# Performance work log

Measured on AMD Instinct MI355X. Metric: run time of the kernel, lower is better.

The kernel has to match this reference:

```python
import jax, jax.numpy as jnp
import numpy as np

N, IN_F, OUT_F = 10000, 512, 64
ALPHA = 0.2       # leaky relu slope
THRESHOLD = 0.01  # hub threshold
NEG_INF = -9.0e15


def setup_inputs() -> dict:
    key = jax.random.key(0)
    k_h, k_adj, k_hub, k_W, k_as, k_ad = jax.random.split(key, 6)
    h = jax.random.normal(k_h, (N, IN_F), dtype=jnp.float32)
    adj = jax.random.randint(k_adj, (N, N), 0, 2, dtype=jnp.int32)
    hub_mask = jax.random.uniform(k_hub, (N,), dtype=jnp.float32)
    # xavier-uniform-ish params (gain 1.414)
    lim_W = 1.414 * np.sqrt(6.0 / (IN_F + OUT_F))
    W = jax.random.uniform(k_W, (IN_F, OUT_F), minval=-lim_W, maxval=lim_W, dtype=jnp.float32)
    lim_a = 1.414 * np.sqrt(6.0 / (OUT_F + 1))
    a_src = jax.random.uniform(k_as, (OUT_F, 1), minval=-lim_a, maxval=lim_a, dtype=jnp.float32)
    a_dst = jax.random.uniform(k_ad, (OUT_F, 1), minval=-lim_a, maxval=lim_a, dtype=jnp.float32)
    return {"h": h, "W": W, "a_src": a_src, "a_dst": a_dst, "hub_mask": hub_mask, "adj": adj}


def reference(h, W, a_src, a_dst, hub_mask, adj):
    Wh = h @ W                                  # [N, F_out]
    e_src = Wh @ a_src                          # [N, 1]
    e_dst = Wh @ a_dst                          # [N, 1]
    e = jax.nn.leaky_relu(e_src + e_dst.T, negative_slope=ALPHA)  # [N, N]
    scores = jnp.where(adj > 0, e, jnp.float32(NEG_INF))
    attention = jax.nn.softmax(scores, axis=1)  # row-wise softmax over neighbors
    attention = jax.nn.relu(attention - hub_mask * THRESHOLD)  # hub threshold prune
    # dropout omitted (inference mode / p applied as no-op for deterministic reference)
    h_prime = attention @ Wh                    # [N, F_out]
    return jax.nn.elu(h_prime)                  # concat=True branch
```

## Files before the change

kernel.cpp:

```cpp
#include <hip/hip_runtime.h>
#include <math.h>

#define N_NODES 10000
#define IN_FEAT 512
#define OUT_FEAT 64
#define LRELU_ALPHA 0.2f
#define HUB_THRESH 0.01f
#define BITS_WORDS 320
#define CAND_CAP 1024

#define WH_OFF   0
#define ESRC_OFF 640000
#define EDST_OFF 650000
#define T_OFF    660000
#define LT_OFF   670000

__global__ __launch_bounds__(256) void k1_gemm(
    const float* __restrict__ h, const float* __restrict__ W,
    const float* __restrict__ a_src, const float* __restrict__ a_dst,
    const float* __restrict__ hub, float* __restrict__ ws)
{
    const int bx = blockIdx.x, tid = threadIdx.x;
    if (bx >= 625) {
        const int base = (bx - 625) * 1024;
        #pragma unroll
        for (int e = 0; e < 4; ++e) {
            int idx = base + e * 256 + tid;
            if (idx < N_NODES) {
                float t = hub[idx] * HUB_THRESH;
                ws[T_OFF + idx]  = t;
                ws[LT_OFF + idx] = logf(t);
            }
        }
        return;
    }

    __shared__ __align__(16) float Ws[64 * 64];
    __shared__ __align__(16) float Hs[16 * 64];
    const int col = tid & 63, rg = tid >> 6;
    const int rowBase = bx * 16;
    float acc[4] = {0.f, 0.f, 0.f, 0.f};

    for (int k0 = 0; k0 < IN_FEAT; k0 += 64) {
        for (int idx = tid; idx < 4096; idx += 256) {
            int kk = idx >> 6, c = idx & 63;
            Ws[idx] = W[(size_t)(k0 + kk) * 64 + c];
        }
        for (int idx = tid; idx < 1024; idx += 256) {
            int r = idx >> 6, kk = idx & 63;
            Hs[idx] = h[(size_t)(rowBase + r) * IN_FEAT + k0 + kk];
        }
        __syncthreads();
        #pragma unroll
        for (int k4 = 0; k4 < 16; ++k4) {
            float4 hv0 = *(const float4*)&Hs[(rg + 0)  * 64 + k4 * 4];
            float4 hv1 = *(const float4*)&Hs[(rg + 4)  * 64 + k4 * 4];
            float4 hv2 = *(const float4*)&Hs[(rg + 8)  * 64 + k4 * 4];
            float4 hv3 = *(const float4*)&Hs[(rg + 12) * 64 + k4 * 4];
            float w0 = Ws[(k4 * 4 + 0) * 64 + col];
            float w1 = Ws[(k4 * 4 + 1) * 64 + col];
            float w2 = Ws[(k4 * 4 + 2) * 64 + col];
            float w3 = Ws[(k4 * 4 + 3) * 64 + col];
            acc[0] += hv0.x * w0 + hv0.y * w1 + hv0.z * w2 + hv0.w * w3;
            acc[1] += hv1.x * w0 + hv1.y * w1 + hv1.z * w2 + hv1.w * w3;
            acc[2] += hv2.x * w0 + hv2.y * w1 + hv2.z * w2 + hv2.w * w3;
            acc[3] += hv3.x * w0 + hv3.y * w1 + hv3.z * w2 + hv3.w * w3;
        }
        __syncthreads();
    }

    const float asv = a_src[col], adv = a_dst[col];
    #pragma unroll
    for (int r = 0; r < 4; ++r) {
        int row = rowBase + rg + 4 * r;
        ws[WH_OFF + (size_t)row * 64 + col] = acc[r];
        float s1 = acc[r] * asv, s2 = acc[r] * adv;
        #pragma unroll
        for (int m = 32; m; m >>= 1) {
            s1 += __shfl_xor(s1, m, 64);
            s2 += __shfl_xor(s2, m, 64);
        }
        if (col == 0) {
            ws[ESRC_OFF + row] = s1;
            ws[EDST_OFF + row] = s2;
        }
    }
}

__global__ __launch_bounds__(256) void k2_fused(
    const int* __restrict__ adj, const float* __restrict__ ws,
    float* __restrict__ out)
{
    const int i = blockIdx.x, tid = threadIdx.x;
    const int lane = tid & 63, w = tid >> 6;
    __shared__ unsigned bits[BITS_WORDS];
    __shared__ float partA[4];
    __shared__ float partB[256];
    __shared__ int   candj[2][CAND_CAP];
    __shared__ float candw[2][CAND_CAP];
    __shared__ int   cnt[10];

    const float esrc = ws[ESRC_OFF + i];
    const float* __restrict__ edst = ws + EDST_OFF;
    const int4* __restrict__ arow = (const int4*)(adj + (size_t)i * N_NODES);
    float acc = 0.f;

    if (tid < 10) cnt[tid] = 0;

    #pragma unroll
    for (int it = 0; it < 10; ++it) {
        const int j0 = it * 1024 + tid * 4;
        unsigned nib = 0;
        if (j0 < N_NODES) {
            int4 a4  = arow[j0 >> 2];
            float4 e4 = *(const float4*)(edst + j0);
            float s, e;
            s = esrc + e4.x; e = fmaxf(s, LRELU_ALPHA * s);
            if (a4.x > 0) { acc += __expf(e); nib |= 1u; }
            s = esrc + e4.y; e = fmaxf(s, LRELU_ALPHA * s);
            if (a4.y > 0) { acc += __expf(e); nib |= 2u; }
            s = esrc + e4.z; e = fmaxf(s, LRELU_ALPHA * s);
            if (a4.z > 0) { acc += __expf(e); nib |= 4u; }
            s = esrc + e4.w; e = fmaxf(s, LRELU_ALPHA * s);
            if (a4.w > 0) { acc += __expf(e); nib |= 8u; }
        }
        unsigned v = nib << ((lane & 7) * 4);
        v |= (unsigned)__shfl_xor((int)v, 1, 64);
        v |= (unsigned)__shfl_xor((int)v, 2, 64);
        v |= (unsigned)__shfl_xor((int)v, 4, 64);
        if ((lane & 7) == 0) bits[j0 >> 5] = v;
    }

    #pragma unroll
    for (int m = 32; m; m >>= 1) acc += __shfl_xor(acc, m, 64);
    if (lane == 0) partA[w] = acc;
    __syncthreads();
    const float l = partA[0] + partA[1] + partA[2] + partA[3];

    const bool empty = (l == 0.0f);
    const float cl = empty ? 0.0f : logf(l);
    const float invN = 1.0f / (float)N_NODES;
    const float thr = cl - 0.0625f;
    const float* __restrict__ tarr  = ws + T_OFF;
    const float* __restrict__ ltarr = ws + LT_OFF;
    const float* __restrict__ Wh    = ws + WH_OFF;
    float oacc = 0.f;

    for (int it = 0; it < 10; ++it) {
        const int buf = it & 1;
        const int j0 = it * 1024 + tid * 4;
        if (j0 < N_NODES) {
            if (!empty) {
                const unsigned word = bits[j0 >> 5];
                const unsigned nib = (word >> (j0 & 31)) & 0xFu;
                if (nib) {
                    float4 e4  = *(const float4*)(edst + j0);
                    float4 lt4 = *(const float4*)(ltarr + j0);
                    #pragma unroll
                    for (int c = 0; c < 4; ++c) {
                        if (nib & (1u << c)) {
                            float ed = (c == 0) ? e4.x : (c == 1) ? e4.y : (c == 2) ? e4.z : e4.w;
                            float lt = (c == 0) ? lt4.x : (c == 1) ? lt4.y : (c == 2) ? lt4.z : lt4.w;
                            float s = esrc + ed;
                            float e = fmaxf(s, LRELU_ALPHA * s);
                            if (e > thr + lt) {
                                float p = __expf(e - cl);
                                float wgt = p - tarr[j0 + c];
                                if (wgt > 0.0f) {
                                    int k = atomicAdd(&cnt[it], 1);
                                    candj[buf][k] = j0 + c;
                                    candw[buf][k] = wgt;
                                }
                            }
                        }
                    }
                }
            } else {
                float4 t4 = *(const float4*)(tarr + j0);
                #pragma unroll
                for (int c = 0; c < 4; ++c) {
                    float tv = (c == 0) ? t4.x : (c == 1) ? t4.y : (c == 2) ? t4.z : t4.w;
                    float wgt = invN - tv;
                    if (wgt > 0.0f) {
                        int k = atomicAdd(&cnt[it], 1);
                        candj[buf][k] = j0 + c;
                        candw[buf][k] = wgt;
                    }
                }
            }
        }
        __syncthreads();
        const int M = cnt[it];
        for (int c = w; c < M; c += 4) {
            int   jj = candj[buf][c];
            float wv = candw[buf][c];
            oacc += wv * Wh[(size_t)jj * 64 + lane];
        }
    }

    partB[tid] = oacc;
    __syncthreads();
    if (w == 0) {
        float tot = partB[lane] + partB[64 + lane] + partB[128 + lane] + partB[192 + lane];
        out[(size_t)i * 64 + lane] = tot > 0.0f ? tot : expm1f(tot);
    }
}

extern "C" void kernel_launch(void* const* d_in, const int* in_sizes, int n_in,
                              void* d_out, int out_size, void* d_ws, size_t ws_size,
                              hipStream_t stream)
{
    const float* h     = (const float*)d_in[0];
    const float* W     = (const float*)d_in[1];
    const float* a_src = (const float*)d_in[2];
    const float* a_dst = (const float*)d_in[3];
    const float* hub   = (const float*)d_in[4];
    const int*   adj   = (const int*)d_in[5];
    float* ws  = (float*)d_ws;
    float* out = (float*)d_out;

    k1_gemm<<<635, 256, 0, stream>>>(h, W, a_src, a_dst, hub, ws);
    k2_fused<<<N_NODES, 256, 0, stream>>>(adj, ws, out);
}
```

Measured before the change: 655.1 us.

## Process two attention rows per block to share edst, threshold and Wh loads

Each block of the fused softmax/aggregation kernel now handles two adjacent rows, so the edst, log-threshold and threshold vectors are loaded once for both rows, and the grid is halved. Candidate index and weight are packed into one int2 array, and the candidate buffers are single-buffered with an extra barrier per iteration. The intent is to amortise the per-row shared vector traffic and block launch overhead. In exchange, per-block register and shared-memory use grows and there are half as many blocks.

```diff
diff --git a/kernel.cpp b/kernel.cpp
--- a/kernel.cpp
+++ b/kernel.cpp
@@ -91,118 +91,162 @@
     const int* __restrict__ adj, const float* __restrict__ ws,
     float* __restrict__ out)
 {
-    const int i = blockIdx.x, tid = threadIdx.x;
+    const int b = blockIdx.x, tid = threadIdx.x;
     const int lane = tid & 63, w = tid >> 6;
-    __shared__ unsigned bits[BITS_WORDS];
-    __shared__ float partA[4];
-    __shared__ float partB[256];
-    __shared__ int   candj[2][CAND_CAP];
-    __shared__ float candw[2][CAND_CAP];
-    __shared__ int   cnt[10];
-
-    const float esrc = ws[ESRC_OFF + i];
+    const int i0 = 2 * b, i1 = 2 * b + 1;
+    __shared__ unsigned bits[2][BITS_WORDS];
+    __shared__ float partA[2][4];
+    __shared__ int2  cand[2][CAND_CAP];
+    __shared__ int   cnt[2][10];
+
+    const float esrc0 = ws[ESRC_OFF + i0];
+    const float esrc1 = ws[ESRC_OFF + i1];
     const float* __restrict__ edst = ws + EDST_OFF;
-    const int4* __restrict__ arow = (const int4*)(adj + (size_t)i * N_NODES);
-    float acc = 0.f;
-
-    if (tid < 10) cnt[tid] = 0;
-
-    #pragma unroll
+    const int4* __restrict__ arow0 = (const int4*)(adj + (size_t)i0 * N_NODES);
+    const int4* __restrict__ arow1 = (const int4*)(adj + (size_t)i1 * N_NODES);
+    float acc0 = 0.f, acc1 = 0.f;
+
+    if (tid < 20) ((int*)cnt)[tid] = 0;
+
+    #pragma unroll 2
     for (int it = 0; it < 10; ++it) {
         const int j0 = it * 1024 + tid * 4;
-        unsigned nib = 0;
+        unsigned nib0 = 0, nib1 = 0;
         if (j0 < N_NODES) {
-            int4 a4  = arow[j0 >> 2];
+            int4 a0 = arow0[j0 >> 2];
+            int4 a1 = arow1[j0 >> 2];
             float4 e4 = *(const float4*)(edst + j0);
             float s, e;
-            s = esrc + e4.x; e = fmaxf(s, LRELU_ALPHA * s);
-            if (a4.x > 0) { acc += __expf(e); nib |= 1u; }
-            s = esrc + e4.y; e = fmaxf(s, LRELU_ALPHA * s);
-            if (a4.y > 0) { acc += __expf(e); nib |= 2u; }
-            s = esrc + e4.z; e = fmaxf(s, LRELU_ALPHA * s);
-            if (a4.z > 0) { acc += __expf(e); nib |= 4u; }
-            s = esrc + e4.w; e = fmaxf(s, LRELU_ALPHA * s);
-            if (a4.w > 0) { acc += __expf(e); nib |= 8u; }
-        }
-        unsigned v = nib << ((lane & 7) * 4);
-        v |= (unsigned)__shfl_xor((int)v, 1, 64);
-        v |= (unsigned)__shfl_xor((int)v, 2, 64);
-        v |= (unsigned)__shfl_xor((int)v, 4, 64);
-        if ((lane & 7) == 0) bits[j0 >> 5] = v;
+            s = esrc0 + e4.x; e = fmaxf(s, LRELU_ALPHA * s);
+            if (a0.x > 0) { acc0 += __expf(e); nib0 |= 1u; }
+            s = esrc0 + e4.y; e = fmaxf(s, LRELU_ALPHA * s);
+            if (a0.y > 0) { acc0 += __expf(e); nib0 |= 2u; }
+            s = esrc0 + e4.z; e = fmaxf(s, LRELU_ALPHA * s);
+            if (a0.z > 0) { acc0 += __expf(e); nib0 |= 4u; }
+            s = esrc0 + e4.w; e = fmaxf(s, LRELU_ALPHA * s);
+            if (a0.w > 0) { acc0 += __expf(e); nib0 |= 8u; }
+            s = esrc1 + e4.x; e = fmaxf(s, LRELU_ALPHA * s);
+            if (a1.x > 0) { acc1 += __expf(e); nib1 |= 1u; }
+            s = esrc1 + e4.y; e = fmaxf(s, LRELU_ALPHA * s);
+            if (a1.y > 0) { acc1 += __expf(e); nib1 |= 2u; }
+            s = esrc1 + e4.z; e = fmaxf(s, LRELU_ALPHA * s);
+            if (a1.z > 0) { acc1 += __expf(e); nib1 |= 4u; }
+            s = esrc1 + e4.w; e = fmaxf(s, LRELU_ALPHA * s);
+            if (a1.w > 0) { acc1 += __expf(e); nib1 |= 8u; }
+        }
+        unsigned v0 = nib0 << ((lane & 7) * 4);
+        unsigned v1 = nib1 << ((lane & 7) * 4);
+        v0 |= (unsigned)__shfl_xor((int)v0, 1, 64);
+        v1 |= (unsigned)__shfl_xor((int)v1, 1, 64);
+        v0 |= (unsigned)__shfl_xor((int)v0, 2, 64);
+        v1 |= (unsigned)__shfl_xor((int)v1, 2, 64);
+        v0 |= (unsigned)__shfl_xor((int)v0, 4, 64);
+        v1 |= (unsigned)__shfl_xor((int)v1, 4, 64);
+        if ((lane & 7) == 0) {
+            bits[0][j0 >> 5] = v0;
+            bits[1][j0 >> 5] = v1;
+        }
     }
 
     #pragma unroll
-    for (int m = 32; m; m >>= 1) acc += __shfl_xor(acc, m, 64);
-    if (lane == 0) partA[w] = acc;
+    for (int m = 32; m; m >>= 1) {
+        acc0 += __shfl_xor(acc0, m, 64);
+        acc1 += __shfl_xor(acc1, m, 64);
+    }
+    if (lane == 0) { partA[0][w] = acc0; partA[1][w] = acc1; }
     __syncthreads();
-    const float l = partA[0] + partA[1] + partA[2] + partA[3];
-
-    const bool empty = (l == 0.0f);
-    const float cl = empty ? 0.0f : logf(l);
+    const float l0 = partA[0][0] + partA[0][1] + partA[0][2] + partA[0][3];
+    const float l1 = partA[1][0] + partA[1][1] + partA[1][2] + partA[1][3];
+
+    const bool empty0 = (l0 == 0.0f), empty1 = (l1 == 0.0f);
+    const float cl0 = empty0 ? 0.0f : logf(l0);
+    const float cl1 = empty1 ? 0.0f : logf(l1);
+    const float thr0 = cl0 - 0.0625f, thr1 = cl1 - 0.0625f;
     const float invN = 1.0f / (float)N_NODES;
-    const float thr = cl - 0.0625f;
     const float* __restrict__ tarr  = ws + T_OFF;
     const float* __restrict__ ltarr = ws + LT_OFF;
     const float* __restrict__ Wh    = ws + WH_OFF;
-    float oacc = 0.f;
+    float oacc0 = 0.f, oacc1 = 0.f;
 
     for (int it = 0; it < 10; ++it) {
-        const int buf = it & 1;
         const int j0 = it * 1024 + tid * 4;
+        unsigned m0 = 0, m1 = 0;
         if (j0 < N_NODES) {
-            if (!empty) {
-                const unsigned word = bits[j0 >> 5];
-                const unsigned nib = (word >> (j0 & 31)) & 0xFu;
-                if (nib) {
-                    float4 e4  = *(const float4*)(edst + j0);
-                    float4 lt4 = *(const float4*)(ltarr + j0);
-                    #pragma unroll
-                    for (int c = 0; c < 4; ++c) {
-                        if (nib & (1u << c)) {
-                            float ed = (c == 0) ? e4.x : (c == 1) ? e4.y : (c == 2) ? e4.z : e4.w;
-                            float lt = (c == 0) ? lt4.x : (c == 1) ? lt4.y : (c == 2) ? lt4.z : lt4.w;
-                            float s = esrc + ed;
-                            float e = fmaxf(s, LRELU_ALPHA * s);
-                            if (e > thr + lt) {
-                                float p = __expf(e - cl);
-                                float wgt = p - tarr[j0 + c];
-                                if (wgt > 0.0f) {
-                                    int k = atomicAdd(&cnt[it], 1);
-                                    candj[buf][k] = j0 + c;
-                                    candw[buf][k] = wgt;
-                                }
-                            }
+            m0 = empty0 ? 0u : (bits[0][j0 >> 5] >> (j0 & 31)) & 0xFu;
+            m1 = empty1 ? 0u : (bits[1][j0 >> 5] >> (j0 & 31)) & 0xFu;
+        }
+        if (m0 | m1) {
+            float4 e4  = *(const float4*)(edst + j0);
+            float4 lt4 = *(const float4*)(ltarr + j0);
+            #pragma unroll
+            for (int c = 0; c < 4; ++c) {
+                float ed = (c == 0) ? e4.x  : (c == 1) ? e4.y  : (c == 2) ? e4.z  : e4.w;
+                float lt = (c == 0) ? lt4.x : (c == 1) ? lt4.y : (c == 2) ? lt4.z : lt4.w;
+                if (m0 & (1u << c)) {
+                    float s = esrc0 + ed;
+                    float e = fmaxf(s, LRELU_ALPHA * s);
+                    if (e > thr0 + lt) {
+                        float p = __expf(e - cl0);
+                        float wgt = p - tarr[j0 + c];
+                        if (wgt > 0.0f) {
+                            int k = atomicAdd(&cnt[0][it], 1);
+                            cand[0][k] = make_int2(j0 + c, __float_as_int(wgt));
                         }
                     }
                 }
-            } else {
-                float4 t4 = *(const float4*)(tarr + j0);
-                #pragma unroll
-                for (int c = 0; c < 4; ++c) {
-                    float tv = (c == 0) ? t4.x : (c == 1) ? t4.y : (c == 2) ? t4.z : t4.w;
-                    float wgt = invN - tv;
-                    if (wgt > 0.0f) {
-                        int k = atomicAdd(&cnt[it], 1);
-                        candj[buf][k] = j0 + c;
-                        candw[buf][k] = wgt;
+                if (m1 & (1u << c)) {
+                    float s = esrc1 + ed;
+                    float e = fmaxf(s, LRELU_ALPHA * s);
+                    if (e > thr1 + lt) {
+                        float p = __expf(e - cl1);
+                        float wgt = p - tarr[j0 + c];
+                        if (wgt > 0.0f) {
+                            int k = atomicAdd(&cnt[1][it], 1);
+                            cand[1][k] = make_int2(j0 + c, __float_as_int(wgt));
+                        }
                     }
                 }
             }
         }
-        __syncthreads();
-        const int M = cnt[it];
-        for (int c = w; c < M; c += 4) {
-            int   jj = candj[buf][c];
-            float wv = candw[buf][c];
-            oacc += wv * Wh[(size_t)jj * 64 + lane];
-        }
-    }
-
-    partB[tid] = oacc;
+        if ((empty0 | empty1) && j0 < N_NODES) {
+            float4 t4 = *(const float4*)(tarr + j0);
+            #pragma unroll
+            for (int c = 0; c < 4; ++c) {
+                float tv = (c == 0) ? t4.x : (c == 1) ? t4.y : (c == 2) ? t4.z : t4.w;
+                float wv = invN - tv;
+                if (wv > 0.0f) {
+                    if (empty0) {
+                        int k = atomicAdd(&cnt[0][it], 1);
+                        cand[0][k] = make_int2(j0 + c, __float_as_int(wv));
+                    }
+                    if (empty1) {
+                        int k = atomicAdd(&cnt[1][it], 1);
+                        cand[1][k] = make_int2(j0 + c, __float_as_int(wv));
+                    }
+                }
+            }
+        }
+        __syncthreads();
+        const int M0 = cnt[0][it], M1 = cnt[1][it];
+        for (int c = w; c < M0; c += 4) {
+            int2 cd = cand[0][c];
+            oacc0 += __int_as_float(cd.y) * Wh[(size_t)cd.x * 64 + lane];
+        }
+        for (int c = w; c < M1; c += 4) {
+            int2 cd = cand[1][c];
+            oacc1 += __int_as_float(cd.y) * Wh[(size_t)cd.x * 64 + lane];
+        }
+        __syncthreads();
+    }
+
+    float* partB = (float*)bits;
+    partB[tid]       = oacc0;
+    partB[256 + tid] = oacc1;
     __syncthreads();
-    if (w == 0) {
-        float tot = partB[lane] + partB[64 + lane] + partB[128 + lane] + partB[192 + lane];
-        out[(size_t)i * 64 + lane] = tot > 0.0f ? tot : expm1f(tot);
+    if (w < 2) {
+        const float* pb = partB + w * 256;
+        float tot = pb[lane] + pb[64 + lane] + pb[128 + lane] + pb[192 + lane];
+        out[(size_t)(i0 + w) * 64 + lane] = tot > 0.0f ? tot : expm1f(tot);
     }
 }
 
@@ -220,5 +264,5 @@
     float* out = (float*)d_out;
 
     k1_gemm<<<635, 256, 0, stream>>>(h, W, a_src, a_dst, hub, ws);
-    k2_fused<<<N_NODES, 256, 0, stream>>>(adj, ws, out);
+    k2_fused<<<N_NODES / 2, 256, 0, stream>>>(adj, ws, out);
 }
```

After: 629.8 us. 3.9% less time.

## Process four attention rows per block to reuse edst/threshold loads

Applied to the files above, without the earlier changes.

Each block of the fused softmax/aggregation kernel now handles four rows instead of one. The edst, log-threshold and threshold vectors are loaded once and reused across the four rows, and there are a quarter as many blocks. The candidate buffers are packed into int2 and capped per row, with an atomic fallback into a shared accumulator on overflow. The main cost is the 400MB adjacency read, which is unchanged, so the gain relies on fewer blocks and less redundant traffic, paid for with more registers and an extra barrier per iteration.

```diff
diff --git a/kernel.cpp b/kernel.cpp
--- a/kernel.cpp
+++ b/kernel.cpp
@@ -7,7 +7,8 @@
 #define LRELU_ALPHA 0.2f
 #define HUB_THRESH 0.01f
 #define BITS_WORDS 320
-#define CAND_CAP 1024
+#define ROWS_PB 4
+#define CAND_CAP 512
 
 #define WH_OFF   0
 #define ESRC_OFF 640000
@@ -91,118 +92,168 @@
     const int* __restrict__ adj, const float* __restrict__ ws,
     float* __restrict__ out)
 {
-    const int i = blockIdx.x, tid = threadIdx.x;
+    const int b = blockIdx.x, tid = threadIdx.x;
     const int lane = tid & 63, w = tid >> 6;
-    __shared__ unsigned bits[BITS_WORDS];
-    __shared__ float partA[4];
-    __shared__ float partB[256];
-    __shared__ int   candj[2][CAND_CAP];
-    __shared__ float candw[2][CAND_CAP];
-    __shared__ int   cnt[10];
-
-    const float esrc = ws[ESRC_OFF + i];
+    const int i0 = ROWS_PB * b;
+    __shared__ unsigned bits[ROWS_PB][BITS_WORDS];
+    __shared__ float partA[ROWS_PB][4];
+    __shared__ int2  cand[ROWS_PB][CAND_CAP];
+    __shared__ int   cnt[ROWS_PB][10];
+    __shared__ float oaccL[ROWS_PB][64];
+
     const float* __restrict__ edst = ws + EDST_OFF;
-    const int4* __restrict__ arow = (const int4*)(adj + (size_t)i * N_NODES);
-    float acc = 0.f;
-
-    if (tid < 10) cnt[tid] = 0;
-
-    #pragma unroll
+    float esrc[ROWS_PB];
+    const int4* arow[ROWS_PB];
+    float acc[ROWS_PB];
+    #pragma unroll
+    for (int r = 0; r < ROWS_PB; ++r) {
+        esrc[r] = ws[ESRC_OFF + i0 + r];
+        arow[r] = (const int4*)(adj + (size_t)(i0 + r) * N_NODES);
+        acc[r] = 0.f;
+    }
+    if (tid < ROWS_PB * 10) ((int*)cnt)[tid] = 0;
+    ((float*)oaccL)[tid] = 0.f;
+
+    #pragma unroll 2
     for (int it = 0; it < 10; ++it) {
         const int j0 = it * 1024 + tid * 4;
-        unsigned nib = 0;
+        unsigned nib[ROWS_PB] = {0, 0, 0, 0};
         if (j0 < N_NODES) {
-            int4 a4  = arow[j0 >> 2];
             float4 e4 = *(const float4*)(edst + j0);
-            float s, e;
-            s = esrc + e4.x; e = fmaxf(s, LRELU_ALPHA * s);
-            if (a4.x > 0) { acc += __expf(e); nib |= 1u; }
-            s = esrc + e4.y; e = fmaxf(s, LRELU_ALPHA * s);
-            if (a4.y > 0) { acc += __expf(e); nib |= 2u; }
-            s = esrc + e4.z; e = fmaxf(s, LRELU_ALPHA * s);
-            if (a4.z > 0) { acc += __expf(e); nib |= 4u; }
-            s = esrc + e4.w; e = fmaxf(s, LRELU_ALPHA * s);
-            if (a4.w > 0) { acc += __expf(e); nib |= 8u; }
-        }
-        unsigned v = nib << ((lane & 7) * 4);
-        v |= (unsigned)__shfl_xor((int)v, 1, 64);
-        v |= (unsigned)__shfl_xor((int)v, 2, 64);
-        v |= (unsigned)__shfl_xor((int)v, 4, 64);
-        if ((lane & 7) == 0) bits[j0 >> 5] = v;
-    }
-
-    #pragma unroll
-    for (int m = 32; m; m >>= 1) acc += __shfl_xor(acc, m, 64);
-    if (lane == 0) partA[w] = acc;
+            float s0 = 0, s1 = 0, s2 = 0, s3 = 0;
+            #pragma unroll
+            for (int r = 0; r < ROWS_PB; ++r) {
+                int4 a4 = arow[r][j0 >> 2];
+                float s, e;
+                s = esrc[r] + e4.x; e = fmaxf(s, LRELU_ALPHA * s);
+                if (a4.x > 0) { acc[r] += __expf(e); nib[r] |= 1u; }
+                s = esrc[r] + e4.y; e = fmaxf(s, LRELU_ALPHA * s);
+                if (a4.y > 0) { acc[r] += __expf(e); nib[r] |= 2u; }
+                s = esrc[r] + e4.z; e = fmaxf(s, LRELU_ALPHA * s);
+                if (a4.z > 0) { acc[r] += __expf(e); nib[r] |= 4u; }
+                s = esrc[r] + e4.w; e = fmaxf(s, LRELU_ALPHA * s);
+                if (a4.w > 0) { acc[r] += __expf(e); nib[r] |= 8u; }
+            }
+            (void)s0; (void)s1; (void)s2; (void)s3;
+        }
+        #pragma unroll
+        for (int r = 0; r < ROWS_PB; ++r) {
+            unsigned v = nib[r] << ((lane & 7) * 4);
+            v |= (unsigned)__shfl_xor((int)v, 1, 64);
+            v |= (unsigned)__shfl_xor((int)v, 2, 64);
+            v |= (unsigned)__shfl_xor((int)v, 4, 64);
+            if ((lane & 7) == 0) bits[r][j0 >> 5] = v;
+        }
+    }
+
+    #pragma unroll
+    for (int r = 0; r < ROWS_PB; ++r) {
+        float a = acc[r];
+        #pragma unroll
+        for (int m = 32; m; m >>= 1) a += __shfl_xor(a, m, 64);
+        if (lane == 0) partA[r][w] = a;
+    }
     __syncthreads();
-    const float l = partA[0] + partA[1] + partA[2] + partA[3];
-
-    const bool empty = (l == 0.0f);
-    const float cl = empty ? 0.0f : logf(l);
+
+    float l[ROWS_PB], cl[ROWS_PB], thr[ROWS_PB];
+    bool empty[ROWS_PB];
+    bool anyEmpty = false;
+    #pragma unroll
+    for (int r = 0; r < ROWS_PB; ++r) {
+        l[r] = partA[r][0] + partA[r][1] + partA[r][2] + partA[r][3];
+        empty[r] = (l[r] == 0.0f);
+        anyEmpty |= empty[r];
+        cl[r] = empty[r] ? 0.0f : logf(l[r]);
+        thr[r] = cl[r] - 0.0625f;
+    }
     const float invN = 1.0f / (float)N_NODES;
-    const float thr = cl - 0.0625f;
     const float* __restrict__ tarr  = ws + T_OFF;
     const float* __restrict__ ltarr = ws + LT_OFF;
     const float* __restrict__ Wh    = ws + WH_OFF;
-    float oacc = 0.f;
+    float oacc[ROWS_PB] = {0.f, 0.f, 0.f, 0.f};
 
     for (int it = 0; it < 10; ++it) {
-        const int buf = it & 1;
         const int j0 = it * 1024 + tid * 4;
+        unsigned m[ROWS_PB] = {0, 0, 0, 0};
         if (j0 < N_NODES) {
-            if (!empty) {
-                const unsigned word = bits[j0 >> 5];
-                const unsigned nib = (word >> (j0 & 31)) & 0xFu;
-                if (nib) {
-                    float4 e4  = *(const float4*)(edst + j0);
-                    float4 lt4 = *(const float4*)(ltarr + j0);
-                    #pragma unroll
-                    for (int c = 0; c < 4; ++c) {
-                        if (nib & (1u << c)) {
-                            float ed = (c == 0) ? e4.x : (c == 1) ? e4.y : (c == 2) ? e4.z : e4.w;
-                            float lt = (c == 0) ? lt4.x : (c == 1) ? lt4.y : (c == 2) ? lt4.z : lt4.w;
-                            float s = esrc + ed;
-                            float e = fmaxf(s, LRELU_ALPHA * s);
-                            if (e > thr + lt) {
-                                float p = __expf(e - cl);
-                                float wgt = p - tarr[j0 + c];
-                                if (wgt > 0.0f) {
-                                    int k = atomicAdd(&cnt[it], 1);
-                                    candj[buf][k] = j0 + c;
-                                    candw[buf][k] = wgt;
+            #pragma unroll
+            for (int r = 0; r < ROWS_PB; ++r)
+                m[r] = empty[r] ? 0u : (bits[r][j0 >> 5] >> (j0 & 31)) & 0xFu;
+        }
+        if (m[0] | m[1] | m[2] | m[3]) {
+            float4 e4  = *(const float4*)(edst + j0);
+            float4 lt4 = *(const float4*)(ltarr + j0);
+            #pragma unroll
+            for (int c = 0; c < 4; ++c) {
+                float ed = (c == 0) ? e4.x  : (c == 1) ? e4.y  : (c == 2) ? e4.z  : e4.w;
+                float lt = (c == 0) ? lt4.x : (c == 1) ? lt4.y : (c == 2) ? lt4.z : lt4.w;
+                #pragma unroll
+                for (int r = 0; r < ROWS_PB; ++r) {
+                    if (m[r] & (1u << c)) {
+                        float s = esrc[r] + ed;
+                        float e = fmaxf(s, LRELU_ALPHA * s);
+                        if (e > thr[r] + lt) {
+                            float p = __expf(e - cl[r]);
+                            float wgt = p - tarr[j0 + c];
+                            if (wgt > 0.0f) {
+                                int k = atomicAdd(&cnt[r][it], 1);
+                                if (k < CAND_CAP) {
+                                    cand[r][k] = make_int2(j0 + c, __float_as_int(wgt));
+                                } else {
+                                    const float* whp = Wh + (size_t)(j0 + c) * 64;
+                                    for (int cc = 0; cc < 64; ++cc)
+                                        atomicAdd(&oaccL[r][cc], wgt * whp[cc]);
                                 }
                             }
                         }
                     }
                 }
-            } else {
-                float4 t4 = *(const float4*)(tarr + j0);
-                #pragma unroll
-                for (int c = 0; c < 4; ++c) {
-                    float tv = (c == 0) ? t4.x : (c == 1) ? t4.y : (c == 2) ? t4.z : t4.w;
-                    float wgt = invN - tv;
-                    if (wgt > 0.0f) {
-                        int k = atomicAdd(&cnt[it], 1);
-                        candj[buf][k] = j0 + c;
-                        candw[buf][k] = wgt;
+            }
+        }
+        if (anyEmpty && j0 < N_NODES) {
+            float4 t4 = *(const float4*)(tarr + j0);
+            #pragma unroll
+            for (int c = 0; c < 4; ++c) {
+                float tv = (c == 0) ? t4.x : (c == 1) ? t4.y : (c == 2) ? t4.z : t4.w;
+                float wv = invN - tv;
+                if (wv > 0.0f) {
+                    #pragma unroll
+                    for (int r = 0; r < ROWS_PB; ++r) {
+                        if (empty[r]) {
+                            int k = atomicAdd(&cnt[r][it], 1);
+                            if (k < CAND_CAP) {
+                                cand[r][k] = make_int2(j0 + c, __float_as_int(wv));
+                            } else {
+                                const float* whp = Wh + (size_t)(j0 + c) * 64;
+                                for (int cc = 0; cc < 64; ++cc)
+                                    atomicAdd(&oaccL[r][cc], wv * whp[cc]);
+                            }
+                        }
                     }
                 }
             }
         }
         __syncthreads();
-        const int M = cnt[it];
-        for (int c = w; c < M; c += 4) {
-            int   jj = candj[buf][c];
-            float wv = candw[buf][c];
-            oacc += wv * Wh[(size_t)jj * 64 + lane];
-        }
-    }
-
-    partB[tid] = oacc;
+        #pragma unroll
+        for (int r = 0; r < ROWS_PB; ++r) {
+            const int M = min(cnt[r][it], CAND_CAP);
+            for (int c = w; c < M; c += 4) {
+                int2 cd = cand[r][c];
+                oacc[r] += __int_as_float(cd.y) * Wh[(size_t)cd.x * 64 + lane];
+            }
+        }
+        __syncthreads();
+    }
+
+    float* partB = (float*)bits;
+    #pragma unroll
+    for (int r = 0; r < ROWS_PB; ++r) partB[r * 256 + tid] = oacc[r];
     __syncthreads();
-    if (w == 0) {
-        float tot = partB[lane] + partB[64 + lane] + partB[128 + lane] + partB[192 + lane];
-        out[(size_t)i * 64 + lane] = tot > 0.0f ? tot : expm1f(tot);
+    {
+        const float* pb = partB + w * 256;
+        float tot = pb[lane] + pb[64 + lane] + pb[128 + lane] + pb[192 + lane]
+                  + oaccL[w][lane];
+        out[(size_t)(i0 + w) * 64 + lane] = tot > 0.0f ? tot : expm1f(tot);
     }
 }
 
@@ -220,5 +271,5 @@
     float* out = (float*)d_out;
 
     k1_gemm<<<635, 256, 0, stream>>>(h, W, a_src, a_dst, hub, ws);
-    k2_fused<<<N_NODES, 256, 0, stream>>>(adj, ws, out);
+    k2_fused<<<N_NODES / ROWS_PB, 256, 0, stream>>>(adj, ws, out);
 }
```

Result: no change. 666.0 us (+1.7%).
